# Optimization experiments

Hardware: AMD Instinct MI355X
Metric: run time of the kernel (lower is better)

Reference implementation:

```python
import jax, jax.numpy as jnp
import numpy as np
from jax import lax

B_SZ = 64
D_MODEL = 768
D_INNER = 1536   # expand * d_model
D_STATE = 16
D_CONV = 4
DT_RANK = 48     # ceil(768/16)
ROWS, COLS = 16, 16
L = ROWS * COLS
LN_EPS = 1e-5


def setup_inputs() -> dict:
    key = jax.random.key(0)
    ks = jax.random.split(key, 16)
    def nrm(k, shape, s):
        return jax.random.normal(k, shape, jnp.float32) * s
    # A_log init as in Mamba: log(arange(1..d_state)) tiled over d_inner
    A_log = jnp.log(jnp.tile(jnp.arange(1, D_STATE + 1, dtype=jnp.float32)[None, :], (D_INNER, 1)))
    # dt bias init: inverse-softplus of dt ~ LogUniform(1e-3, 1e-1)
    def dt_bias_init(k):
        u = jax.random.uniform(k, (D_INNER,), jnp.float32)
        dt = jnp.exp(u * (np.log(0.1) - np.log(0.001)) + np.log(0.001))
        return dt + jnp.log(-jnp.expm1(-dt))
    dt_std = DT_RANK ** -0.5
    return {
        "hidden_states": jax.random.normal(ks[0], (B_SZ, L, D_MODEL), jnp.float32),
        "in_proj_w": nrm(ks[1], (2 * D_INNER, D_MODEL), 0.02),
        "conv_w": nrm(ks[2], (D_INNER, D_CONV), 0.2),
        "conv_bias": nrm(ks[3], (D_INNER,), 0.1),
        "conv_w_b": nrm(ks[4], (D_INNER, D_CONV), 0.2),
        "conv_bias_b": nrm(ks[5], (D_INNER,), 0.1),
        "x_proj_w": nrm(ks[6], (DT_RANK + 2 * D_STATE, D_INNER), 0.02),
        "x_proj_w_b": nrm(ks[7], (DT_RANK + 2 * D_STATE, D_INNER), 0.02),
        "dt_proj_w": jax.random.uniform(ks[8], (D_INNER, DT_RANK), jnp.float32, -dt_std, dt_std),
        "dt_proj_w_b": jax.random.uniform(ks[9], (D_INNER, DT_RANK), jnp.float32, -dt_std, dt_std),
        "dt_bias": dt_bias_init(ks[10]),
        "dt_bias_b": dt_bias_init(ks[11]),
        "A_log": A_log,
        "A_b_log": A_log,
        "Dp": jnp.ones((D_INNER,), jnp.float32),
        "Dp_b": jnp.ones((D_INNER,), jnp.float32),
        "ln_gamma": jnp.ones((D_INNER,), jnp.float32),
        "ln_beta": jnp.zeros((D_INNER,), jnp.float32),
        "out_proj_w": nrm(ks[12], (D_MODEL, D_INNER), 0.02),
    }


def _causal_conv_silu(x, w, b):
    # x: (B, D, L); depthwise causal conv (left-pad K-1) + SiLU
    y = lax.conv_general_dilated(x, w[:, None, :], (1,), [(D_CONV - 1, 0)],
                                 dimension_numbers=("NCH", "OIH", "NCH"),
                                 feature_group_count=D_INNER)
    return jax.nn.silu(y + b[None, :, None])


def _selective_scan(u, dt, A_log, Bm, Cm, dt_bias):
    # u, dt: (B, D, Lr); Bm, Cm: (B, N, Lr)
    A = -jnp.exp(A_log)                                     # (D, N)
    delta = jax.nn.softplus(dt + dt_bias[None, :, None])    # (B, D, Lr)
    dA = jnp.exp(jnp.einsum("bdl,dn->lbdn", delta, A))     # (Lr, B, D, N)
    dBu = jnp.einsum("bdl,bnl,bdl->lbdn", delta, Bm, u)    # (Lr, B, D, N)
    C_l = jnp.moveaxis(Cm, -1, 0)                           # (Lr, B, N)
    def step(h, inp):
        dA_t, dBu_t, C_t = inp
        h = dA_t * h + dBu_t
        return h, jnp.einsum("bdn,bn->bd", h, C_t)
    h0 = jnp.zeros(dA.shape[1:], dA.dtype)
    _, ys = lax.scan(step, h0, (dA, dBu, C_l))
    return jnp.moveaxis(ys, 0, -1)                          # (B, D, Lr)


def _direction(x, conv_w, conv_bias, x_proj_w, dt_proj_w, dt_bias, A_log, Dp):
    xc = _causal_conv_silu(x, conv_w, conv_bias)            # (B, D, L)
    x_comp = xc.reshape(-1, D_INNER, ROWS, COLS).mean(axis=3)  # (B, D, ROWS)
    x_dbl = jnp.einsum("bdl,ed->ble", x_comp, x_proj_w)    # (B, ROWS, R+2N)
    dt, Bm, Cm = jnp.split(x_dbl, [DT_RANK, DT_RANK + D_STATE], axis=-1)
    dt = jnp.einsum("blr,dr->bdl", dt, dt_proj_w)          # (B, D, ROWS)
    Bm = jnp.moveaxis(Bm, 1, 2)                             # (B, N, ROWS)
    Cm = jnp.moveaxis(Cm, 1, 2)
    y = _selective_scan(x_comp, dt, A_log, Bm, Cm, dt_bias)
    return jnp.repeat(y, COLS, axis=2) + Dp[None, :, None] * xc  # (B, D, L)


def reference(hidden_states, in_proj_w, conv_w, conv_bias, conv_w_b, conv_bias_b,
              x_proj_w, x_proj_w_b, dt_proj_w, dt_proj_w_b, dt_bias, dt_bias_b,
              A_log, A_b_log, Dp, Dp_b, ln_gamma, ln_beta, out_proj_w):
    xz = jnp.einsum("bld,ed->bel", hidden_states, in_proj_w)  # (B, 2*Di, L)
    x, z = jnp.split(xz, 2, axis=1)
    out_f = _direction(x, conv_w, conv_bias, x_proj_w, dt_proj_w, dt_bias, A_log, Dp)
    out_b = _direction(x[:, :, ::-1], conv_w_b, conv_bias_b, x_proj_w_b, dt_proj_w_b, dt_bias_b, A_b_log, Dp_b)
    comb = jnp.moveaxis((out_f + out_b[:, :, ::-1]) * 0.5, 1, 2)  # (B, L, Di)
    mu = comb.mean(-1, keepdims=True)
    var = comb.var(-1, keepdims=True)
    normed = (comb - mu) * lax.rsqrt(var + LN_EPS) * ln_gamma + ln_beta
    gated = normed * jax.nn.silu(jnp.moveaxis(z, 1, 2))
    return jnp.einsum("bld,od->blo", gated, out_proj_w)       # (B, L, d_model)
```

## Files before the change

kernel.cpp:

```cpp
#include <hip/hip_runtime.h>
#include <cstdint>
#include <cstddef>

typedef __bf16 bf16_t;
typedef __attribute__((ext_vector_type(2))) __bf16 bf16x2;
typedef __attribute__((ext_vector_type(4))) __bf16 bf16x4;
typedef __attribute__((ext_vector_type(8))) __bf16 bf16x8;
typedef __attribute__((ext_vector_type(4))) float f32x4;
typedef __attribute__((ext_vector_type(2))) float f32x2;

#define NB     64
#define LSEQ   256
#define DM     768
#define DI     1536
#define NSTATE 16
#define NROWS  16
#define RANK   48

#define BF16_PROBE 0x3F803F80u

__device__ __forceinline__ float bf2f(bf16_t v) { return (float)v; }

__device__ __forceinline__ float ldp(const void* p, size_t i, bool isbf) {
  return isbf ? (float)((const bf16_t*)p)[i] : ((const float*)p)[i];
}

__device__ __forceinline__ float silu_f(float x) {
  const float e = __expf(-fabsf(x));
  return (x >= 0.f) ? (x / (1.f + e)) : (x * e / (1.f + e));
}

__device__ __forceinline__ void async16(const bf16_t* g, bf16_t* l) {
  __builtin_amdgcn_global_load_lds(
      (const __attribute__((address_space(1))) void*)g,
      (__attribute__((address_space(3))) void*)l, 16, 0, 0);
}

__device__ __forceinline__ void cvt8(const void* in, bf16_t* out, int i, bool isbf) {
  if (isbf) {
    ((bf16x8*)out)[i] = ((const bf16x8*)in)[i];
  } else {
    const float* f = (const float*)in + (size_t)i * 8;
    f32x4 lo = *(const f32x4*)f, hi = *(const f32x4*)(f + 4);
    ((bf16x8*)out)[i] = (bf16x8){(bf16_t)lo.x, (bf16_t)lo.y, (bf16_t)lo.z, (bf16_t)lo.w,
                                 (bf16_t)hi.x, (bf16_t)hi.y, (bf16_t)hi.z, (bf16_t)hi.w};
  }
}

#define P_CWF   0
#define P_CWB   6144
#define P_CBF   12288
#define P_CBB   13824
#define P_DP    15360
#define P_DPB   16896
#define P_GAM   18432
#define P_BET   19968
#define P_DTBF  21504
#define P_DTBB  23040
#define P_DTWTF 24576
#define P_DTWTB 98304
#define P_TOTAL 172032

#define PREP_NH    6144
#define PREP_NWIN  1152
#define PREP_NWOUT 576
#define PREP_NPAR  672
__global__ __launch_bounds__(256) void prep_kernel(
    const void* __restrict__ H, const void* __restrict__ Win,
    const void* __restrict__ Wout,
    const void* __restrict__ cw_f, const void* __restrict__ cw_b,
    const void* __restrict__ cb_f, const void* __restrict__ cb_b,
    const void* __restrict__ Dp, const void* __restrict__ Dp_b,
    const void* __restrict__ gam, const void* __restrict__ bet,
    const void* __restrict__ dtb_f, const void* __restrict__ dtb_b,
    const void* __restrict__ dtw_f, const void* __restrict__ dtw_b,
    bf16_t* __restrict__ Hb, bf16_t* __restrict__ Winb, bf16_t* __restrict__ Woutb,
    float* __restrict__ P,
    const uint32_t* __restrict__ probe)
{
  const bool isbf = (probe[0] == BF16_PROBE);
  int blk = blockIdx.x;
  if (blk < PREP_NH) {
    cvt8(H, Hb, blk * 256 + threadIdx.x, isbf);
  } else if (blk < PREP_NH + PREP_NWIN) {
    cvt8(Win, Winb, (blk - PREP_NH) * 256 + threadIdx.x, isbf);
  } else if (blk < PREP_NH + PREP_NWIN + PREP_NWOUT) {
    cvt8(Wout, Woutb, (blk - PREP_NH - PREP_NWIN) * 256 + threadIdx.x, isbf);
  } else {
    const int p = (blk - PREP_NH - PREP_NWIN - PREP_NWOUT) * 256 + (int)threadIdx.x;
    float v;
    if (p < P_CWB)            v = ldp(cw_f, p, isbf);
    else if (p < P_CBF)       v = ldp(cw_b, p - P_CWB, isbf);
    else if (p < P_CBB)       v = ldp(cb_f, p - P_CBF, isbf);
    else if (p < P_DP)        v = ldp(cb_b, p - P_CBB, isbf);
    else if (p < P_DPB)       v = ldp(Dp,   p - P_DP, isbf);
    else if (p < P_GAM)       v = ldp(Dp_b, p - P_DPB, isbf);
    else if (p < P_BET)       v = ldp(gam,  p - P_GAM, isbf);
    else if (p < P_DTBF)      v = ldp(bet,  p - P_BET, isbf);
    else if (p < P_DTBB)      v = ldp(dtb_f, p - P_DTBF, isbf);
    else if (p < P_DTWTF)     v = ldp(dtb_b, p - P_DTBB, isbf);
    else if (p < P_DTWTB) {
      const int q = p - P_DTWTF, r = q / DI, d = q - r * DI;
      v = ldp(dtw_f, (size_t)d * RANK + r, isbf);
    } else {
      const int q = p - P_DTWTB, r = q / DI, d = q - r * DI;
      v = ldp(dtw_b, (size_t)d * RANK + r, isbf);
    }
    P[p] = v;
  }
}

#define LDS_IDX(ab, db, half) (((ab) << 2) + ((db) << 1) + (half))

#define STAGE(ab, db, half, kt) do {                                          \
    const int _kt = ((kt) < NT) ? (kt) : (NT - 1);                            \
    const bf16_t* _g = (ab) ? B : A;                                          \
    const size_t _rb = ((ab) ? bn : bm) + (size_t)((half) * 128);             \
    bf16_t* _l = &sm[LDS_IDX(ab, db, half)][0];                               \
    _Pragma("unroll")                                                         \
    for (int _j = 0; _j < 2; _j++) {                                          \
      const int _c = wave * 2 + _j;                                           \
      async16(_g + (_rb + _c * 8 + srow) * (size_t)K + (size_t)_kt * 64 + scol,\
              _l + _c * 512);                                                 \
    }                                                                         \
  } while (0)

#define LOAD_A(db, mg) do {                                                   \
    _Pragma("unroll")                                                         \
    for (int _t = 0; _t < 2; _t++) {                                          \
      const int _mt = (mg) * 2 + _t;                                          \
      const int _lr = _mt * 32 + wm * 16 + r;                                 \
      const bf16_t* _b = &sm[LDS_IDX(0, db, _mt >> 2)][(_lr & 127) * 64];     \
      _Pragma("unroll")                                                       \
      for (int _s = 0; _s < 2; _s++)                                          \
        af[_t][_s] = *(const bf16x8*)&_b[(((_s * 4 + quad) ^ r7) * 8)];       \
    }                                                                         \
  } while (0)

#define LOAD_B(db) do {                                                       \
    _Pragma("unroll")                                                         \
    for (int _nt = 0; _nt < 4; _nt++) {                                       \
      const int _lr = _nt * 64 + wn * 16 + r;                                 \
      const bf16_t* _b = &sm[LDS_IDX(1, db, _lr >> 7)][(_lr & 127) * 64];     \
      _Pragma("unroll")                                                       \
      for (int _s = 0; _s < 2; _s++)                                          \
        bfr[_nt][_s] = *(const bf16x8*)&_b[(((_s * 4 + quad) ^ r7) * 8)];     \
    }                                                                         \
  } while (0)

#define MFMA16(mg) do {                                                       \
    __builtin_amdgcn_s_setprio(1);                                            \
    _Pragma("unroll")                                                         \
    for (int _t = 0; _t < 2; _t++)                                            \
    _Pragma("unroll")                                                         \
    for (int _nt = 0; _nt < 4; _nt++)                                         \
    _Pragma("unroll")                                                         \
    for (int _s = 0; _s < 2; _s++)                                            \
      acc[(mg) * 2 + _t][_nt] = __builtin_amdgcn_mfma_f32_16x16x32_bf16(      \
          af[_t][_s], bfr[_nt][_s], acc[(mg) * 2 + _t][_nt], 0, 0, 0);        \
    __builtin_amdgcn_s_setprio(0);                                            \
  } while (0)

#define BAR()    __builtin_amdgcn_s_barrier()
#define WAITL0() asm volatile("s_waitcnt lgkmcnt(0)" ::: "memory")
#define WAITV6() asm volatile("s_waitcnt vmcnt(6)" ::: "memory")

__global__ __launch_bounds__(512, 2) void gemm256_kernel(
    const bf16_t* __restrict__ A, const bf16_t* __restrict__ B,
    void* __restrict__ C, int M, int N, int K, int mode,
    bf16_t* __restrict__ xb)
{
  __shared__ bf16_t sm[8][8192];
  const int tid  = threadIdx.x;
  const int wave = tid >> 6, lane = tid & 63;
  const int wm = wave >> 2, wn = wave & 3;
  const int r = lane & 15, quad = lane >> 4, r7 = lane & 7;
  const int srow = lane >> 3;
  const int scol = ((lane & 7) ^ srow) * 8;
  const int NT = K >> 6;

  const int nwg  = gridDim.x * gridDim.y;
  const int orig = blockIdx.y * gridDim.x + blockIdx.x;
  const int swz  = (orig & 7) * (nwg >> 3) + (orig >> 3);
  const size_t bm = (size_t)(swz / gridDim.x) * 256;
  const size_t bn = (size_t)(swz % gridDim.x) * 256;

  f32x4 acc[8][4];
#pragma unroll
  for (int i = 0; i < 8; i++)
#pragma unroll
    for (int j = 0; j < 4; j++) acc[i][j] = (f32x4){0.f, 0.f, 0.f, 0.f};

  bf16x8 af[2][2];
  bf16x8 bfr[4][2];

  STAGE(1, 0, 0, 0);  STAGE(1, 0, 1, 0);  STAGE(0, 0, 0, 0);  STAGE(0, 0, 1, 0);
  asm volatile("s_waitcnt vmcnt(4)" ::: "memory");
  STAGE(1, 1, 0, 1);  STAGE(1, 1, 1, 1);  STAGE(0, 1, 0, 1);
  WAITV6();
  BAR();

  const int NP = NT >> 1;
  for (int i = 0; i < NP; ++i) {
    const int t1 = 2 * i + 1, t2 = 2 * i + 2, t3 = 2 * i + 3;
    LOAD_B(0); LOAD_A(0, 0); STAGE(0, 1, 1, t1);
    BAR(); WAITL0(); MFMA16(0); BAR();

    LOAD_A(0, 1); STAGE(1, 0, 0, t2);
    BAR(); WAITL0(); MFMA16(1); BAR();

    LOAD_A(0, 2); STAGE(1, 0, 1, t2);
    BAR(); WAITL0(); MFMA16(2); BAR();

    LOAD_A(0, 3); STAGE(0, 0, 0, t2);
    WAITV6();
    BAR(); WAITL0(); MFMA16(3); BAR();

    LOAD_B(1); LOAD_A(1, 0); STAGE(0, 0, 1, t2);
    BAR(); WAITL0(); MFMA16(0); BAR();

    LOAD_A(1, 1); STAGE(1, 1, 0, t3);
    BAR(); WAITL0(); MFMA16(1); BAR();

    LOAD_A(1, 2); STAGE(1, 1, 1, t3);
    BAR(); WAITL0(); MFMA16(2); BAR();

    LOAD_A(1, 3); STAGE(0, 1, 0, t3);
    WAITV6();
    BAR(); WAITL0(); MFMA16(3); BAR();
  }

  const int col16 = lane & 15;
  const int rb4 = quad * 4;

  if (mode == 0) {
#pragma unroll
    for (int mt = 0; mt < 8; mt++)
#pragma unroll
      for (int nt = 0; nt < 4; nt++)
#pragma unroll
        for (int v = 0; v < 4; v++) {
          const size_t m = bm + mt * 32 + wm * 16 + rb4 + v;
          const size_t n = bn + nt * 64 + wn * 16 + col16;
          ((float*)C)[m * (size_t)N + n] = acc[mt][nt][v];
        }
  } else {
    bf16_t* dst = (bn < (size_t)DI) ? xb : (bf16_t*)C;
    const size_t cb0 = (bn < (size_t)DI) ? bn : bn - DI;
#pragma unroll
    for (int mt = 0; mt < 8; mt++)
#pragma unroll
      for (int nt = 0; nt < 4; nt++)
#pragma unroll
        for (int v = 0; v < 4; v++) {
          const size_t m = bm + mt * 32 + wm * 16 + rb4 + v;
          dst[m * DI + cb0 + nt * 64 + wn * 16 + col16] = (bf16_t)acc[mt][nt][v];
        }
  }
}

__global__ __launch_bounds__(384) void conv_kernel(
    const bf16_t* __restrict__ xb, const float* __restrict__ P,
    bf16_t* __restrict__ xc_f, bf16_t* __restrict__ xc_b,
    float* __restrict__ comp_f, float* __restrict__ comp_b)
{
  const int bi = blockIdx.x;
  const int chunk = bi & 7;
  const int b = bi >> 3;
  const int d0 = (int)threadIdx.x * 4;
  const int lr0 = chunk * 32;

  f32x4 wf[4], wb_[4];
#pragma unroll
  for (int c = 0; c < 4; c++) {
    wf[c]  = *(const f32x4*)&P[P_CWF + (d0 + c) * 4];
    wb_[c] = *(const f32x4*)&P[P_CWB + (d0 + c) * 4];
  }
  const f32x4 cbf = *(const f32x4*)&P[P_CBF + d0];
  const f32x4 cbb = *(const f32x4*)&P[P_CBB + d0];

  const bf16_t* xrow = xb + (size_t)b * LSEQ * DI + d0;

  float t0[4], t1[4], t2[4], t3[4];
#pragma unroll
  for (int c = 0; c < 4; c++) { t0[c] = t1[c] = t2[c] = t3[c] = 0.f; }
  if (lr0 > 0) {
    const bf16x4 h1 = *(const bf16x4*)&xrow[(size_t)(lr0 - 3) * DI];
    const bf16x4 h2 = *(const bf16x4*)&xrow[(size_t)(lr0 - 2) * DI];
    const bf16x4 h3 = *(const bf16x4*)&xrow[(size_t)(lr0 - 1) * DI];
#pragma unroll
    for (int c = 0; c < 4; c++) { t1[c] = (float)h1[c]; t2[c] = (float)h2[c]; t3[c] = (float)h3[c]; }
  }

  float sf[4] = {0.f, 0.f, 0.f, 0.f};
  float sb[4] = {0.f, 0.f, 0.f, 0.f};
  for (int l = lr0; l < lr0 + 35; ++l) {
    float xv[4] = {0.f, 0.f, 0.f, 0.f};
    if (l < LSEQ) {
      const bf16x4 v = *(const bf16x4*)&xrow[(size_t)l * DI];
#pragma unroll
      for (int c = 0; c < 4; c++) xv[c] = (float)v[c];
    }
#pragma unroll
    for (int c = 0; c < 4; c++) { t0[c] = t1[c]; t1[c] = t2[c]; t2[c] = t3[c]; t3[c] = xv[c]; }

    if (l < lr0 + 32) {
      bf16x4 yo;
      float y[4];
#pragma unroll
      for (int c = 0; c < 4; c++) {
        y[c] = silu_f(cbf[c] + wf[c].x * t0[c] + wf[c].y * t1[c] + wf[c].z * t2[c] + wf[c].w * t3[c]);
        yo[c] = (bf16_t)y[c];
        sf[c] += y[c];
      }
      *(bf16x4*)&xc_f[((size_t)b * LSEQ + l) * DI + d0] = yo;
      if ((l & 15) == 15) {
        *(f32x4*)&comp_f[((size_t)b * NROWS + (l >> 4)) * DI + d0] =
            (f32x4){sf[0] * (1.f / 16.f), sf[1] * (1.f / 16.f),
                    sf[2] * (1.f / 16.f), sf[3] * (1.f / 16.f)};
#pragma unroll
        for (int c = 0; c < 4; c++) sf[c] = 0.f;
      }
    }
    if (l >= lr0 + 3) {
      const int j = 258 - l;
      bf16x4 yo;
      float y[4];
#pragma unroll
      for (int c = 0; c < 4; c++) {
        y[c] = silu_f(cbb[c] + wb_[c].x * t3[c] + wb_[c].y * t2[c] + wb_[c].z * t1[c] + wb_[c].w * t0[c]);
        yo[c] = (bf16_t)y[c];
        sb[c] += y[c];
      }
      *(bf16x4*)&xc_b[((size_t)b * LSEQ + j) * DI + d0] = yo;
      if ((j & 15) == 0) {
        *(f32x4*)&comp_b[((size_t)b * NROWS + (j >> 4)) * DI + d0] =
            (f32x4){sb[0] * (1.f / 16.f), sb[1] * (1.f / 16.f),
                    sb[2] * (1.f / 16.f), sb[3] * (1.f / 16.f)};
#pragma unroll
        for (int c = 0; c < 4; c++) sb[c] = 0.f;
      }
    }
  }
}

__global__ __launch_bounds__(256) void xproj_kernel(
    const float* __restrict__ comp_f, const float* __restrict__ comp_b,
    const void* __restrict__ w_f, const void* __restrict__ w_b,
    float* __restrict__ xd_f, float* __restrict__ xd_b,
    const uint32_t* __restrict__ probe)
{
  const bool isbf = (probe[0] == BF16_PROBE);
  const int dir = blockIdx.y;
  const int rg = blockIdx.x;
  const float* comp = dir ? comp_b : comp_f;
  const void* W = dir ? w_b : w_f;
  float* out = dir ? xd_b : xd_f;
  const int r0 = rg * 8;

  __shared__ float xs[8][DI];
  for (int i = threadIdx.x; i < 8 * DI; i += 256)
    xs[i / DI][i % DI] = comp[(size_t)r0 * DI + i];
  __syncthreads();

  const int wave = threadIdx.x >> 6, lane = threadIdx.x & 63;
  for (int oo = 0; oo < 20; ++oo) {
    const int o = wave * 20 + oo;
    float a[8];
#pragma unroll
    for (int rr = 0; rr < 8; rr++) a[rr] = 0.f;
#pragma unroll
    for (int j = 0; j < 24; ++j) {
      const int k = lane + 64 * j;
      const float wv = ldp(W, (size_t)o * DI + k, isbf);
#pragma unroll
      for (int rr = 0; rr < 8; rr++) a[rr] += xs[rr][k] * wv;
    }
    for (int off = 32; off; off >>= 1) {
#pragma unroll
      for (int rr = 0; rr < 8; rr++) a[rr] += __shfl_down(a[rr], off);
    }
    if (lane == 0) {
#pragma unroll
      for (int rr = 0; rr < 8; rr++) out[(size_t)(r0 + rr) * 80 + o] = a[rr];
    }
  }
}

__global__ __launch_bounds__(256) void scan_kernel(
    const float* __restrict__ xd_fg, const float* __restrict__ xd_bg,
    const float* comp_f, const float* comp_b,
    const float* __restrict__ P,
    const void* __restrict__ Al_f, const void* __restrict__ Al_b,
    float* y_fg, float* y_bg,
    const uint32_t* __restrict__ probe)
{
  const bool isbf = (probe[0] == BF16_PROBE);
  const int dir = blockIdx.y;
  const int b = blockIdx.x / 6;
  const int d = (blockIdx.x % 6) * 256 + threadIdx.x;
  const float* xd_g = dir ? xd_bg : xd_fg;
  const float* comp = dir ? comp_b : comp_f;
  const float* dtwT = P + (dir ? P_DTWTB : P_DTWTF);
  const float bias = P[(dir ? P_DTBB : P_DTBF) + d];
  const void* Al  = dir ? Al_b : Al_f;
  float* y = dir ? y_bg : y_fg;

  __shared__ float xd[NROWS * 80];
  for (int i = threadIdx.x; i < NROWS * 80; i += 256) xd[i] = xd_g[(size_t)b * (NROWS * 80) + i];
  __syncthreads();

  float dt[NROWS];
#pragma unroll
  for (int l = 0; l < NROWS; l++) dt[l] = 0.f;
  for (int r = 0; r < RANK; r++) {
    const float w = dtwT[(size_t)r * DI + d];
#pragma unroll
    for (int l = 0; l < NROWS; l++) dt[l] += xd[l * 80 + r] * w;
  }

  float A[NSTATE];
#pragma unroll
  for (int n = 0; n < NSTATE; n++) A[n] = -__expf(ldp(Al, (size_t)d * NSTATE + n, isbf));

  float h[NSTATE];
#pragma unroll
  for (int n = 0; n < NSTATE; n++) h[n] = 0.f;

  for (int l = 0; l < NROWS; l++) {
    const float u = comp[((size_t)b * NROWS + l) * DI + d];
    const float dv = dt[l] + bias;
    const float delta = (dv > 15.f) ? dv : log1pf(__expf(dv));
    const float du = delta * u;
    float yv = 0.f;
#pragma unroll
    for (int n = 0; n < NSTATE; n++) {
      const float hn = __expf(delta * A[n]) * h[n] + du * xd[l * 80 + RANK + n];
      h[n] = hn;
      yv += hn * xd[l * 80 + RANK + NSTATE + n];
    }
    y[((size_t)b * NROWS + l) * DI + d] = yv;
  }
}

__global__ __launch_bounds__(384) void combine_kernel(
    const float* __restrict__ y_f, const float* __restrict__ y_b,
    bf16_t* xcg_f,
    const bf16_t* __restrict__ xc_b,
    const bf16_t* __restrict__ zb,
    const float* __restrict__ P)
{
  const int m = blockIdx.x;
  const int b = m >> 8, l = m & 255;
  const int lr = LSEQ - 1 - l;
  const int tid = threadIdx.x;
  const int wave = tid >> 6, lane = tid & 63;
  const int d0 = tid * 4;

  const bf16x4 cfv = *(const bf16x4*)&xcg_f[((size_t)b * LSEQ + l) * DI + d0];
  const bf16x4 cbv = *(const bf16x4*)&xc_b[((size_t)b * LSEQ + lr) * DI + d0];
  const f32x4 yfv = *(const f32x4*)&y_f[((size_t)b * NROWS + (l >> 4)) * DI + d0];
  const f32x4 ybv = *(const f32x4*)&y_b[((size_t)b * NROWS + (lr >> 4)) * DI + d0];
  const f32x4 dp  = *(const f32x4*)&P[P_DP + d0];
  const f32x4 dpb = *(const f32x4*)&P[P_DPB + d0];

  float v[4];
  float sum = 0.f, sq = 0.f;
#pragma unroll
  for (int c = 0; c < 4; c++) {
    const float cc = 0.5f * ((yfv[c] + dp[c] * (float)cfv[c]) +
                             (ybv[c] + dpb[c] * (float)cbv[c]));
    v[c] = cc; sum += cc; sq += cc * cc;
  }
  for (int off = 32; off; off >>= 1) {
    sum += __shfl_down(sum, off);
    sq  += __shfl_down(sq, off);
  }
  __shared__ float rs[6], rq[6];
  if (lane == 0) { rs[wave] = sum; rq[wave] = sq; }
  __syncthreads();
  float S = 0.f, SQ = 0.f;
#pragma unroll
  for (int w = 0; w < 6; w++) { S += rs[w]; SQ += rq[w]; }
  const float mu = S * (1.f / (float)DI);
  const float var = fmaxf(SQ * (1.f / (float)DI) - mu * mu, 0.f);
  const float rstd = rsqrtf(var + 1e-5f);

  const f32x4 gm = *(const f32x4*)&P[P_GAM + d0];
  const f32x4 bt = *(const f32x4*)&P[P_BET + d0];
  const bf16x4 zv = *(const bf16x4*)&zb[(size_t)m * DI + d0];
  bf16x4 outv;
#pragma unroll
  for (int c = 0; c < 4; c++) {
    const float nrm = (v[c] - mu) * rstd * gm[c] + bt[c];
    outv[c] = (bf16_t)(nrm * silu_f((float)zv[c]));
  }
  *(bf16x4*)&xcg_f[(size_t)m * DI + d0] = outv;
}

extern "C" void kernel_launch(void* const* d_in, const int* in_sizes, int n_in,
                              void* d_out, int out_size, void* d_ws, size_t ws_size,
                              hipStream_t stream)
{
  (void)in_sizes; (void)n_in; (void)out_size; (void)ws_size;
  const void* H     = d_in[0];
  const void* Win   = d_in[1];
  const void* cw_f  = d_in[2];
  const void* cb_f  = d_in[3];
  const void* cw_b  = d_in[4];
  const void* cb_b  = d_in[5];
  const void* xpw_f = d_in[6];
  const void* xpw_b = d_in[7];
  const void* dtw_f = d_in[8];
  const void* dtw_b = d_in[9];
  const void* dtb_f = d_in[10];
  const void* dtb_b = d_in[11];
  const void* Al_f  = d_in[12];
  const void* Al_b  = d_in[13];
  const void* Dp    = d_in[14];
  const void* Dp_b  = d_in[15];
  const void* gam   = d_in[16];
  const void* bet   = d_in[17];
  const void* Wout  = d_in[18];
  const uint32_t* probe = (const uint32_t*)d_in[14];

  const size_t M = (size_t)NB * LSEQ;
  char* ws = (char*)d_ws;
  bf16_t* zb    = (bf16_t*)ws;  ws += M * DI * sizeof(bf16_t);
  bf16_t* xb    = (bf16_t*)ws;  ws += M * DI * sizeof(bf16_t);
  bf16_t* xc_f  = (bf16_t*)ws;  ws += M * DI * sizeof(bf16_t);
  bf16_t* xc_b  = (bf16_t*)ws;  ws += M * DI * sizeof(bf16_t);
  float* comp_f = (float*)ws;   ws += (size_t)NB * NROWS * DI * sizeof(float);
  float* comp_b = (float*)ws;   ws += (size_t)NB * NROWS * DI * sizeof(float);
  float* xd_f   = (float*)ws;   ws += (size_t)NB * NROWS * 80 * sizeof(float);
  float* xd_b   = (float*)ws;   ws += (size_t)NB * NROWS * 80 * sizeof(float);
  bf16_t* Hb    = (bf16_t*)ws;  ws += M * DM * sizeof(bf16_t);
  bf16_t* Winb  = (bf16_t*)ws;  ws += (size_t)(2 * DI) * DM * sizeof(bf16_t);
  bf16_t* Woutb = (bf16_t*)ws;  ws += (size_t)DM * DI * sizeof(bf16_t);
  float* P      = (float*)ws;   ws += (size_t)P_TOTAL * sizeof(float);

  prep_kernel<<<PREP_NH + PREP_NWIN + PREP_NWOUT + PREP_NPAR, 256, 0, stream>>>(
      H, Win, Wout, cw_f, cw_b, cb_f, cb_b, Dp, Dp_b, gam, bet,
      dtb_f, dtb_b, dtw_f, dtw_b, Hb, Winb, Woutb, P, probe);

  gemm256_kernel<<<dim3(2 * DI / 256, M / 256), 512, 0, stream>>>(
      Hb, Winb, zb, (int)M, 2 * DI, DM, 1, xb);

  conv_kernel<<<dim3(512), 384, 0, stream>>>(
      xb, P, xc_f, xc_b, comp_f, comp_b);

  xproj_kernel<<<dim3(128, 2), 256, 0, stream>>>(
      comp_f, comp_b, xpw_f, xpw_b, xd_f, xd_b, probe);

  scan_kernel<<<dim3(NB * (DI / 256), 2), 256, 0, stream>>>(
      xd_f, xd_b, comp_f, comp_b, P, Al_f, Al_b, comp_f, comp_b, probe);

  combine_kernel<<<dim3(NB * LSEQ), 384, 0, stream>>>(
      comp_f, comp_b, xc_f, xc_b, zb, P);

  gemm256_kernel<<<dim3(DM / 256, M / 256), 512, 0, stream>>>(
      xc_f, Woutb, d_out, (int)M, DM, DI, 0, nullptr);
}
```

Measured before the change: 452.9 us.

## Fuse x-projection into selective scan kernel and swizzle combine block order

The separate x-projection and scan kernels become one kernel per (batch, direction). Each block stages all 16 compressed rows in LDS, computes the 80 projected outputs into shared memory, then runs the dt projection and scan over three 512-channel chunks. This removes one launch and the global round trip for the projected values. The cost is only 128 large blocks with about 100KB of LDS each, which reduces parallelism in the scan phase. Separately, the combine kernel's block index is remapped so that blocks sharing the same y row groups run near each other, to improve cache reuse.

```diff
diff --git a/kernel.cpp b/kernel.cpp
--- a/kernel.cpp
+++ b/kernel.cpp
@@ -344,52 +344,9 @@
   }
 }
 
-__global__ __launch_bounds__(256) void xproj_kernel(
+__global__ __launch_bounds__(512) void xscan_kernel(
     const float* __restrict__ comp_f, const float* __restrict__ comp_b,
     const void* __restrict__ w_f, const void* __restrict__ w_b,
-    float* __restrict__ xd_f, float* __restrict__ xd_b,
-    const uint32_t* __restrict__ probe)
-{
-  const bool isbf = (probe[0] == BF16_PROBE);
-  const int dir = blockIdx.y;
-  const int rg = blockIdx.x;
-  const float* comp = dir ? comp_b : comp_f;
-  const void* W = dir ? w_b : w_f;
-  float* out = dir ? xd_b : xd_f;
-  const int r0 = rg * 8;
-
-  __shared__ float xs[8][DI];
-  for (int i = threadIdx.x; i < 8 * DI; i += 256)
-    xs[i / DI][i % DI] = comp[(size_t)r0 * DI + i];
-  __syncthreads();
-
-  const int wave = threadIdx.x >> 6, lane = threadIdx.x & 63;
-  for (int oo = 0; oo < 20; ++oo) {
-    const int o = wave * 20 + oo;
-    float a[8];
-#pragma unroll
-    for (int rr = 0; rr < 8; rr++) a[rr] = 0.f;
-#pragma unroll
-    for (int j = 0; j < 24; ++j) {
-      const int k = lane + 64 * j;
-      const float wv = ldp(W, (size_t)o * DI + k, isbf);
-#pragma unroll
-      for (int rr = 0; rr < 8; rr++) a[rr] += xs[rr][k] * wv;
-    }
-    for (int off = 32; off; off >>= 1) {
-#pragma unroll
-      for (int rr = 0; rr < 8; rr++) a[rr] += __shfl_down(a[rr], off);
-    }
-    if (lane == 0) {
-#pragma unroll
-      for (int rr = 0; rr < 8; rr++) out[(size_t)(r0 + rr) * 80 + o] = a[rr];
-    }
-  }
-}
-
-__global__ __launch_bounds__(256) void scan_kernel(
-    const float* __restrict__ xd_fg, const float* __restrict__ xd_bg,
-    const float* comp_f, const float* comp_b,
     const float* __restrict__ P,
     const void* __restrict__ Al_f, const void* __restrict__ Al_b,
     float* y_fg, float* y_bg,
@@ -397,49 +354,77 @@
 {
   const bool isbf = (probe[0] == BF16_PROBE);
   const int dir = blockIdx.y;
-  const int b = blockIdx.x / 6;
-  const int d = (blockIdx.x % 6) * 256 + threadIdx.x;
-  const float* xd_g = dir ? xd_bg : xd_fg;
+  const int b = blockIdx.x;
   const float* comp = dir ? comp_b : comp_f;
+  const void* W = dir ? w_b : w_f;
   const float* dtwT = P + (dir ? P_DTWTB : P_DTWTF);
-  const float bias = P[(dir ? P_DTBB : P_DTBF) + d];
-  const void* Al  = dir ? Al_b : Al_f;
+  const float* dtb = P + (dir ? P_DTBB : P_DTBF);
+  const void* Al = dir ? Al_b : Al_f;
   float* y = dir ? y_bg : y_fg;
 
-  __shared__ float xd[NROWS * 80];
-  for (int i = threadIdx.x; i < NROWS * 80; i += 256) xd[i] = xd_g[(size_t)b * (NROWS * 80) + i];
+  __shared__ float cs[NROWS * DI];
+  __shared__ float xds[NROWS][80];
+
+  const float* cg = comp + (size_t)b * NROWS * DI;
+  for (int i = threadIdx.x; i < NROWS * DI; i += 512) cs[i] = cg[i];
   __syncthreads();
 
-  float dt[NROWS];
-#pragma unroll
-  for (int l = 0; l < NROWS; l++) dt[l] = 0.f;
-  for (int r = 0; r < RANK; r++) {
-    const float w = dtwT[(size_t)r * DI + d];
-#pragma unroll
-    for (int l = 0; l < NROWS; l++) dt[l] += xd[l * 80 + r] * w;
-  }
-
-  float A[NSTATE];
-#pragma unroll
-  for (int n = 0; n < NSTATE; n++) A[n] = -__expf(ldp(Al, (size_t)d * NSTATE + n, isbf));
-
-  float h[NSTATE];
-#pragma unroll
-  for (int n = 0; n < NSTATE; n++) h[n] = 0.f;
-
-  for (int l = 0; l < NROWS; l++) {
-    const float u = comp[((size_t)b * NROWS + l) * DI + d];
-    const float dv = dt[l] + bias;
-    const float delta = (dv > 15.f) ? dv : log1pf(__expf(dv));
-    const float du = delta * u;
-    float yv = 0.f;
-#pragma unroll
-    for (int n = 0; n < NSTATE; n++) {
-      const float hn = __expf(delta * A[n]) * h[n] + du * xd[l * 80 + RANK + n];
-      h[n] = hn;
-      yv += hn * xd[l * 80 + RANK + NSTATE + n];
-    }
-    y[((size_t)b * NROWS + l) * DI + d] = yv;
+  const int wave = threadIdx.x >> 6, lane = threadIdx.x & 63;
+  for (int oo = 0; oo < 10; ++oo) {
+    const int o = wave * 10 + oo;
+    float a[NROWS];
+#pragma unroll
+    for (int rr = 0; rr < NROWS; rr++) a[rr] = 0.f;
+#pragma unroll
+    for (int j = 0; j < 24; ++j) {
+      const int k = lane + 64 * j;
+      const float wv = ldp(W, (size_t)o * DI + k, isbf);
+#pragma unroll
+      for (int rr = 0; rr < NROWS; rr++) a[rr] += cs[rr * DI + k] * wv;
+    }
+    for (int off = 32; off; off >>= 1) {
+#pragma unroll
+      for (int rr = 0; rr < NROWS; rr++) a[rr] += __shfl_down(a[rr], off);
+    }
+    if (lane == 0) {
+#pragma unroll
+      for (int rr = 0; rr < NROWS; rr++) xds[rr][o] = a[rr];
+    }
+  }
+  __syncthreads();
+
+  for (int ch = 0; ch < 3; ++ch) {
+    const int d = ch * 512 + (int)threadIdx.x;
+    float dt[NROWS];
+#pragma unroll
+    for (int l = 0; l < NROWS; l++) dt[l] = 0.f;
+    for (int r = 0; r < RANK; r++) {
+      const float w = dtwT[(size_t)r * DI + d];
+#pragma unroll
+      for (int l = 0; l < NROWS; l++) dt[l] += xds[l][r] * w;
+    }
+    float A[NSTATE];
+#pragma unroll
+    for (int n = 0; n < NSTATE; n++) A[n] = -__expf(ldp(Al, (size_t)d * NSTATE + n, isbf));
+    const float bias = dtb[d];
+    float h[NSTATE];
+#pragma unroll
+    for (int n = 0; n < NSTATE; n++) h[n] = 0.f;
+
+    for (int l = 0; l < NROWS; l++) {
+      const float u = cs[l * DI + d];
+      const float dv = dt[l] + bias;
+      const float delta = (dv > 15.f) ? dv : log1pf(__expf(dv));
+      const float du = delta * u;
+      float yv = 0.f;
+#pragma unroll
+      for (int n = 0; n < NSTATE; n++) {
+        const float hn = __expf(delta * A[n]) * h[n] + du * xds[l][RANK + n];
+        h[n] = hn;
+        yv += hn * xds[l][RANK + NSTATE + n];
+      }
+      y[((size_t)b * NROWS + l) * DI + d] = yv;
+    }
   }
 }
 
@@ -450,7 +435,10 @@
     const bf16_t* __restrict__ zb,
     const float* __restrict__ P)
 {
-  const int m = blockIdx.x;
+  const int bid = blockIdx.x;
+  const int G = (bid >> 7) * 8 + (bid & 7);
+  const int o = (bid >> 3) & 15;
+  const int m = G * 16 + o;
   const int b = m >> 8, l = m & 255;
   const int lr = LSEQ - 1 - l;
   const int tid = threadIdx.x;
@@ -532,8 +520,6 @@
   bf16_t* xc_b  = (bf16_t*)ws;  ws += M * DI * sizeof(bf16_t);
   float* comp_f = (float*)ws;   ws += (size_t)NB * NROWS * DI * sizeof(float);
   float* comp_b = (float*)ws;   ws += (size_t)NB * NROWS * DI * sizeof(float);
-  float* xd_f   = (float*)ws;   ws += (size_t)NB * NROWS * 80 * sizeof(float);
-  float* xd_b   = (float*)ws;   ws += (size_t)NB * NROWS * 80 * sizeof(float);
   bf16_t* Hb    = (bf16_t*)ws;  ws += M * DM * sizeof(bf16_t);
   bf16_t* Winb  = (bf16_t*)ws;  ws += (size_t)(2 * DI) * DM * sizeof(bf16_t);
   bf16_t* Woutb = (bf16_t*)ws;  ws += (size_t)DM * DI * sizeof(bf16_t);
@@ -549,11 +535,8 @@
   conv_kernel<<<dim3(512), 384, 0, stream>>>(
       xb, P, xc_f, xc_b, comp_f, comp_b);
 
-  xproj_kernel<<<dim3(128, 2), 256, 0, stream>>>(
-      comp_f, comp_b, xpw_f, xpw_b, xd_f, xd_b, probe);
-
-  scan_kernel<<<dim3(NB * (DI / 256), 2), 256, 0, stream>>>(
-      xd_f, xd_b, comp_f, comp_b, P, Al_f, Al_b, comp_f, comp_b, probe);
+  xscan_kernel<<<dim3(NB, 2), 512, 0, stream>>>(
+      comp_f, comp_b, xpw_f, xpw_b, P, Al_f, Al_b, comp_f, comp_b, probe);
 
   combine_kernel<<<dim3(NB * LSEQ), 384, 0, stream>>>(
       comp_f, comp_b, xc_f, xc_b, zb, P);
```

Measured after the change: 857.1 us. +89.2%, slower.
